# Kernel optimization log

Measured on AMD Instinct MI355X. Metric: run time of the kernel, lower is better.

Reference implementation:

```python
import jax, jax.numpy as jnp
import numpy as np

NBINS = 29
NODES = 5


def setup_inputs() -> dict:
    key = jax.random.key(0)
    ks = jax.random.split(key, 9)
    B, Tq, Td, V, H = 64, 32, 4096, 100000, 300
    sentence = jax.random.randint(ks[0], (B, Td), 0, V)
    query_sentence = jax.random.randint(ks[1], (B, Tq), 0, V)
    query_idf = jax.random.uniform(ks[2], (B, Tq), jnp.float32)
    emb = jax.random.normal(ks[3], (V, H), jnp.float32)
    w1 = jax.random.uniform(ks[4], (NBINS + 1, NODES), jnp.float32, -0.1, 0.1)
    b1 = jnp.zeros((NODES,), jnp.float32)
    w2 = jax.random.uniform(ks[5], (NODES, 1), jnp.float32, -0.1, 0.1)
    b2 = jnp.zeros((1,), jnp.float32)
    gate_w = jax.random.uniform(ks[6], (1,), jnp.float32, -0.01, 0.01)
    out_w = jax.random.normal(ks[7], (1, 1), jnp.float32) * 0.1
    out_b = jnp.zeros((1,), jnp.float32)
    return dict(sentence=sentence, query_sentence=query_sentence, query_idf=query_idf,
                emb=emb, w1=w1, b1=b1, w2=w2, b2=b2, gate_w=gate_w, out_w=out_w, out_b=out_b)


def reference(sentence, query_sentence, query_idf, emb, w1, b1, w2, b2, gate_w, out_w, out_b):
    B, Td = sentence.shape
    Tq = query_sentence.shape[1]
    q_mask = (query_sentence != 0).astype(jnp.float32)  # (B,Tq)
    d_mask = (sentence != 0).astype(jnp.float32)        # (B,Td)
    qx = emb[query_sentence]                            # (B,Tq,H)
    dx = emb[sentence]                                  # (B,Td,H)
    q_norm = jnp.sqrt(jnp.sum(qx * qx, -1) + 1e-7)[:, :, None] + 1e-7
    d_norm = jnp.sqrt(jnp.sum(dx * dx, -1) + 1e-7)[:, None, :] + 1e-7
    sim = jnp.einsum('bqh,bdh->bqd', qx, dx) / q_norm / d_norm  # (B,Tq,Td)
    sim = sim + (1.0 - d_mask)[:, None, :] * 1e7  # push masked doc positions out of all bins
    # Histogram: original does nbins cumulative (sim < ub) passes then a cumulative
    # subtraction; equivalent per-element bin index + one scatter-add pass.
    ubs = jnp.linspace(-1.0, 1.0, NBINS + 1)[1:]
    idx = jnp.searchsorted(ubs, sim, side='right')  # bin j <=> ub[j-1] <= sim < ub[j]; NBINS = out-of-range
    rows = jnp.arange(B * Tq)[:, None]
    counts = jnp.zeros((B * Tq, NBINS), jnp.float32).at[rows, idx.reshape(B * Tq, Td)].add(1.0, mode='drop')
    counts = counts.reshape(B, Tq, NBINS)
    exact = jnp.sum((sim > 0.999) & (sim < 1.001), axis=-1).astype(jnp.float32)  # exact-match bin
    hist = jnp.log(jnp.concatenate([counts, exact[..., None]], axis=-1) + 1.0)   # histType == 'LCH'
    ffw = jnp.tanh(jnp.tanh(hist @ w1 + b1) @ w2 + b2)[..., 0]  # (B,Tq)
    # gateType == 'IDF': Linear(1,1,bias=False) on idf, masked softmax over query terms
    gate_logits = query_idf * gate_w[0] + (1.0 - q_mask) * -1e7
    w = jax.nn.softmax(gate_logits, axis=1)
    x = jnp.sum(w * ffw, axis=-1, keepdims=True)  # (B,1)
    return x * out_w[0, 0] + out_b
```

## Files before the change

kernel.cpp:

```cpp
#include <hip/hip_runtime.h>
#include <hip/hip_bf16.h>
#include <math.h>

#define B_    64
#define TQ    32
#define TD    4096
#define HDIM  300
#define NB    29
#define NFEAT 30
#define NKT   19
#define THREADS 256
#define DPB   64
#define QF_SLOTS (NKT * 2 * 64)
#define QF_F4    (QF_SLOTS / 2)
#define QF_BYTES (QF_SLOTS * 8)

typedef _Float16 half4 __attribute__((ext_vector_type(4)));
typedef float    f32x4 __attribute__((ext_vector_type(4)));

__device__ __forceinline__ float ubf(int k) {
    return (float)(-1.0 + (2.0 * (double)(k + 1)) / 29.0);
}

__device__ __forceinline__ void bin_one(float sim, unsigned* s_hist, int q) {
    if (sim > 0.999f && sim < 1.001f) {
        atomicAdd(&s_hist[q * NFEAT + 28], 1u);
        atomicAdd(&s_hist[q * NFEAT + 29], 1u);
    } else {
        int idx = (int)((sim + 1.0f) * 14.5f);
        idx = idx < 0 ? 0 : (idx > NB ? NB : idx);
        while (idx < NB && sim >= ubf(idx)) ++idx;
        while (idx > 0 && sim < ubf(idx - 1)) --idx;
        if (idx < NB) atomicAdd(&s_hist[q * NFEAT + idx], 1u);
    }
}

__global__ void k_qfrag(const int* __restrict__ qsent, const float* __restrict__ emb,
                        _Float16* __restrict__ qf, float* __restrict__ invq) {
    const int b = blockIdx.x;
    const int t = threadIdx.x;
    const int row = t & 31, half = t >> 5;
    __shared__ float pn[2][TQ];
    const int tok = qsent[b * TQ + row];
    const float* p = emb + (size_t)tok * HDIM;
    _Float16* qfb = qf + (size_t)b * (QF_SLOTS * 4);
    float n = 0.f;
    for (int i = 0; i < 38; ++i) {
        const int jf = half * 38 + i;
        const int kg = jf * 4;
        float4 v = make_float4(0.f, 0.f, 0.f, 0.f);
        if (kg < 297) v = *(const float4*)(p + kg);
        n = fmaf(v.x, v.x, n); n = fmaf(v.y, v.y, n);
        n = fmaf(v.z, v.z, n); n = fmaf(v.w, v.w, n);
        half4 h = {(_Float16)v.x, (_Float16)v.y, (_Float16)v.z, (_Float16)v.w};
        const int kt = jf >> 2, g = jf & 3;
        const int slot = (kt * 2 + (row >> 4)) * 64 + (row & 15) + 16 * g;
        *(half4*)&qfb[slot * 4] = h;
    }
    pn[half][row] = n;
    __syncthreads();
    if (half == 0) {
        float s = pn[0][row] + pn[1][row];
        invq[b * TQ + row] = 1.0f / (sqrtf(s + 1e-7f) + 1e-7f);
    }
}

__global__ __launch_bounds__(THREADS) void k_main(
        const int* __restrict__ sent, const float* __restrict__ emb,
        const _Float16* __restrict__ qf, const float* __restrict__ invq,
        unsigned* __restrict__ ghist) {
    __shared__ __align__(16) _Float16 afr[QF_SLOTS * 4];
    __shared__ int      toks[DPB];
    __shared__ float    s_iq[TQ];
    __shared__ unsigned s_hist[TQ * NFEAT];

    const int b    = blockIdx.x >> 6;
    const int d0   = (blockIdx.x & 63) * DPB;
    const int tid  = threadIdx.x;
    const int wid  = tid >> 6;
    const int lane = tid & 63;

    if (tid < DPB) toks[tid] = sent[b * TD + d0 + tid];
    if (tid < TQ)  s_iq[tid] = invq[b * TQ + tid];
    for (int i = tid; i < TQ * NFEAT; i += THREADS) s_hist[i] = 0u;
    {
        const float4* qfp = (const float4*)(qf + (size_t)b * (QF_SLOTS * 4));
        float4* afp = (float4*)afr;
        for (int i = tid; i < QF_F4; i += THREADS) afp[i] = qfp[i];
    }
    __syncthreads();

    const int g4   = lane >> 4;
    const int rloc = wid * 16 + (lane & 15);
    const int tok  = toks[rloc];
    const float* bp = emb + (size_t)tok * HDIM + g4 * 4;

    f32x4 acc0 = {0.f, 0.f, 0.f, 0.f};
    f32x4 acc1 = {0.f, 0.f, 0.f, 0.f};
    float nd = 0.f;

    auto ldB = [&](int kt) -> float4 {
        if (kt == 18 && g4 == 3) return make_float4(0.f, 0.f, 0.f, 0.f);
        return *(const float4*)(bp + kt * 16);
    };

    float4 pre[6];
#pragma unroll
    for (int p = 0; p < 6; ++p) pre[p] = ldB(p);

#pragma unroll
    for (int kt = 0; kt < NKT; ++kt) {
        float4 v = pre[kt % 6];
        if (kt + 6 < NKT) pre[kt % 6] = ldB(kt + 6);
        nd = fmaf(v.x, v.x, nd); nd = fmaf(v.y, v.y, nd);
        nd = fmaf(v.z, v.z, nd); nd = fmaf(v.w, v.w, nd);
        half4 hb = {(_Float16)v.x, (_Float16)v.y, (_Float16)v.z, (_Float16)v.w};
        half4 a0 = *(const half4*)&afr[((kt * 2 + 0) * 64 + lane) * 4];
        half4 a1 = *(const half4*)&afr[((kt * 2 + 1) * 64 + lane) * 4];
        acc0 = __builtin_amdgcn_mfma_f32_16x16x16f16(a0, hb, acc0, 0, 0, 0);
        acc1 = __builtin_amdgcn_mfma_f32_16x16x16f16(a1, hb, acc1, 0, 0, 0);
    }

    float s = nd;
    s += __shfl_xor(s, 16, 64);
    s += __shfl_xor(s, 32, 64);
    const float idv = 1.0f / (sqrtf(s + 1e-7f) + 1e-7f);

    if (tok != 0) {
#pragma unroll
        for (int r = 0; r < 4; ++r) {
            const int q0 = g4 * 4 + r;
            bin_one(acc0[r] * s_iq[q0] * idv, s_hist, q0);
            const int q1 = 16 + g4 * 4 + r;
            bin_one(acc1[r] * s_iq[q1] * idv, s_hist, q1);
        }
    }
    __syncthreads();
    for (int i = tid; i < TQ * NFEAT; i += THREADS) {
        unsigned v = s_hist[i];
        if (v) atomicAdd(&ghist[b * TQ * NFEAT + i], v);
    }
}

__global__ void k_finish(const unsigned* __restrict__ ghist,
                         const int* __restrict__ qsent, const float* __restrict__ idf,
                         const float* __restrict__ w1, const float* __restrict__ b1,
                         const float* __restrict__ w2, const float* __restrict__ b2,
                         const float* __restrict__ gw, const float* __restrict__ ow,
                         const float* __restrict__ ob, float* __restrict__ out) {
    int b = blockIdx.x;
    int lane = threadIdx.x;
    float ffw = 0.f;
    float logit = -3.0e38f;
    if (lane < TQ) {
        const unsigned* h = ghist + (b * TQ + lane) * NFEAT;
        float f[NFEAT];
        for (int k = 0; k < NFEAT; ++k) f[k] = logf((float)h[k] + 1.0f);
        float s2 = b2[0];
        for (int n = 0; n < 5; ++n) {
            float s = b1[n];
            for (int k = 0; k < NFEAT; ++k) s = fmaf(f[k], w1[k * 5 + n], s);
            s2 = fmaf(tanhf(s), w2[n], s2);
        }
        ffw = tanhf(s2);
        int qt = qsent[b * TQ + lane];
        logit = idf[b * TQ + lane] * gw[0] + (qt == 0 ? -1e7f : 0.f);
    }
    float m = logit;
#pragma unroll
    for (int t = 1; t < 64; t <<= 1) m = fmaxf(m, __shfl_xor(m, t, 64));
    float e = expf(logit - m);
    float se = e, sw = e * ffw;
#pragma unroll
    for (int t = 1; t < 64; t <<= 1) {
        se += __shfl_xor(se, t, 64);
        sw += __shfl_xor(sw, t, 64);
    }
    if (lane == 0) out[b] = (sw / se) * ow[0] + ob[0];
}

extern "C" void kernel_launch(void* const* d_in, const int* in_sizes, int n_in,
                              void* d_out, int out_size, void* d_ws, size_t ws_size,
                              hipStream_t stream) {
    const int*   sent  = (const int*)d_in[0];
    const int*   qsent = (const int*)d_in[1];
    const float* idf   = (const float*)d_in[2];
    const float* emb   = (const float*)d_in[3];
    const float* w1    = (const float*)d_in[4];
    const float* b1    = (const float*)d_in[5];
    const float* w2    = (const float*)d_in[6];
    const float* b2    = (const float*)d_in[7];
    const float* gw    = (const float*)d_in[8];
    const float* ow    = (const float*)d_in[9];
    const float* ob    = (const float*)d_in[10];
    float* out = (float*)d_out;

    char* ws = (char*)d_ws;
    unsigned*  ghist = (unsigned*)ws;
    _Float16*  qfrag = (_Float16*)(ws + (256 << 10));
    float*     invq  = (float*)(ws + (256 << 10) + (size_t)B_ * QF_BYTES);

    hipMemsetAsync(ghist, 0, (size_t)B_ * TQ * NFEAT * 4, stream);
    k_qfrag<<<B_, 64, 0, stream>>>(qsent, emb, qfrag, invq);
    k_main<<<B_ * (TD / DPB), THREADS, 0, stream>>>(sent, emb, qfrag, invq, ghist);
    k_finish<<<B_, 64, 0, stream>>>(ghist, qsent, idf, w1, b1, w2, b2, gw, ow, ob, out);
}
```

Baseline: 96.32 us.

## Process two doc tile sets per warp and issue gathers before LDS setup

Each block now handles 128 document tokens instead of 64. Each wave processes two 16-row sets, so every LDS load of query fragments feeds twice as many MFMAs. Token ids are read directly from global memory, and the first embedding gathers are issued before the shared-memory histogram clear and query-fragment copy, so load latency overlaps that setup. This halves the grid size and the per-block setup and flush cost, at the price of doubled register use for prefetch buffers and accumulators, which may lower occupancy.

```diff
diff --git a/kernel.cpp b/kernel.cpp
--- a/kernel.cpp
+++ b/kernel.cpp
@@ -10,7 +10,9 @@
 #define NFEAT 30
 #define NKT   19
 #define THREADS 256
-#define DPB   64
+#define DPB   128
+#define NSET  2
+#define RDEP  6
 #define QF_SLOTS (NKT * 2 * 64)
 #define QF_F4    (QF_SLOTS / 2)
 #define QF_BYTES (QF_SLOTS * 8)
@@ -70,69 +72,85 @@
         const _Float16* __restrict__ qf, const float* __restrict__ invq,
         unsigned* __restrict__ ghist) {
     __shared__ __align__(16) _Float16 afr[QF_SLOTS * 4];
-    __shared__ int      toks[DPB];
     __shared__ float    s_iq[TQ];
     __shared__ unsigned s_hist[TQ * NFEAT];
 
-    const int b    = blockIdx.x >> 6;
-    const int d0   = (blockIdx.x & 63) * DPB;
+    const int b    = blockIdx.x >> 5;
+    const int d0   = (blockIdx.x & 31) * DPB;
     const int tid  = threadIdx.x;
     const int wid  = tid >> 6;
     const int lane = tid & 63;
 
-    if (tid < DPB) toks[tid] = sent[b * TD + d0 + tid];
-    if (tid < TQ)  s_iq[tid] = invq[b * TQ + tid];
+    const int g4   = lane >> 4;
+    const int r16  = lane & 15;
+    int tok[NSET];
+    const float* bp[NSET];
+#pragma unroll
+    for (int s = 0; s < NSET; ++s) {
+        tok[s] = sent[b * TD + d0 + wid * 16 + r16 + s * 64];
+        bp[s]  = emb + (size_t)tok[s] * HDIM + g4 * 4;
+    }
+
+    auto ldB = [&](int s, int kt) -> float4 {
+        if (kt == 18 && g4 == 3) return make_float4(0.f, 0.f, 0.f, 0.f);
+        return *(const float4*)(bp[s] + kt * 16);
+    };
+
+    float4 pre[NSET][RDEP];
+#pragma unroll
+    for (int p = 0; p < RDEP; ++p) {
+#pragma unroll
+        for (int s = 0; s < NSET; ++s) pre[s][p] = ldB(s, p);
+    }
+
     for (int i = tid; i < TQ * NFEAT; i += THREADS) s_hist[i] = 0u;
     {
         const float4* qfp = (const float4*)(qf + (size_t)b * (QF_SLOTS * 4));
         float4* afp = (float4*)afr;
         for (int i = tid; i < QF_F4; i += THREADS) afp[i] = qfp[i];
     }
+    if (tid < TQ) s_iq[tid] = invq[b * TQ + tid];
     __syncthreads();
 
-    const int g4   = lane >> 4;
-    const int rloc = wid * 16 + (lane & 15);
-    const int tok  = toks[rloc];
-    const float* bp = emb + (size_t)tok * HDIM + g4 * 4;
-
-    f32x4 acc0 = {0.f, 0.f, 0.f, 0.f};
-    f32x4 acc1 = {0.f, 0.f, 0.f, 0.f};
-    float nd = 0.f;
-
-    auto ldB = [&](int kt) -> float4 {
-        if (kt == 18 && g4 == 3) return make_float4(0.f, 0.f, 0.f, 0.f);
-        return *(const float4*)(bp + kt * 16);
-    };
-
-    float4 pre[6];
-#pragma unroll
-    for (int p = 0; p < 6; ++p) pre[p] = ldB(p);
+    f32x4 acc0[NSET], acc1[NSET];
+    float nd[NSET];
+#pragma unroll
+    for (int s = 0; s < NSET; ++s) {
+        acc0[s] = (f32x4){0.f, 0.f, 0.f, 0.f};
+        acc1[s] = (f32x4){0.f, 0.f, 0.f, 0.f};
+        nd[s] = 0.f;
+    }
 
 #pragma unroll
     for (int kt = 0; kt < NKT; ++kt) {
-        float4 v = pre[kt % 6];
-        if (kt + 6 < NKT) pre[kt % 6] = ldB(kt + 6);
-        nd = fmaf(v.x, v.x, nd); nd = fmaf(v.y, v.y, nd);
-        nd = fmaf(v.z, v.z, nd); nd = fmaf(v.w, v.w, nd);
-        half4 hb = {(_Float16)v.x, (_Float16)v.y, (_Float16)v.z, (_Float16)v.w};
         half4 a0 = *(const half4*)&afr[((kt * 2 + 0) * 64 + lane) * 4];
         half4 a1 = *(const half4*)&afr[((kt * 2 + 1) * 64 + lane) * 4];
-        acc0 = __builtin_amdgcn_mfma_f32_16x16x16f16(a0, hb, acc0, 0, 0, 0);
-        acc1 = __builtin_amdgcn_mfma_f32_16x16x16f16(a1, hb, acc1, 0, 0, 0);
-    }
-
-    float s = nd;
-    s += __shfl_xor(s, 16, 64);
-    s += __shfl_xor(s, 32, 64);
-    const float idv = 1.0f / (sqrtf(s + 1e-7f) + 1e-7f);
-
-    if (tok != 0) {
-#pragma unroll
-        for (int r = 0; r < 4; ++r) {
-            const int q0 = g4 * 4 + r;
-            bin_one(acc0[r] * s_iq[q0] * idv, s_hist, q0);
-            const int q1 = 16 + g4 * 4 + r;
-            bin_one(acc1[r] * s_iq[q1] * idv, s_hist, q1);
+#pragma unroll
+        for (int s = 0; s < NSET; ++s) {
+            float4 v = pre[s][kt % RDEP];
+            if (kt + RDEP < NKT) pre[s][kt % RDEP] = ldB(s, kt + RDEP);
+            nd[s] = fmaf(v.x, v.x, nd[s]); nd[s] = fmaf(v.y, v.y, nd[s]);
+            nd[s] = fmaf(v.z, v.z, nd[s]); nd[s] = fmaf(v.w, v.w, nd[s]);
+            half4 hb = {(_Float16)v.x, (_Float16)v.y, (_Float16)v.z, (_Float16)v.w};
+            acc0[s] = __builtin_amdgcn_mfma_f32_16x16x16f16(a0, hb, acc0[s], 0, 0, 0);
+            acc1[s] = __builtin_amdgcn_mfma_f32_16x16x16f16(a1, hb, acc1[s], 0, 0, 0);
+        }
+    }
+
+#pragma unroll
+    for (int s = 0; s < NSET; ++s) {
+        float t = nd[s];
+        t += __shfl_xor(t, 16, 64);
+        t += __shfl_xor(t, 32, 64);
+        const float idv = 1.0f / (sqrtf(t + 1e-7f) + 1e-7f);
+        if (tok[s] != 0) {
+#pragma unroll
+            for (int r = 0; r < 4; ++r) {
+                const int q0 = g4 * 4 + r;
+                bin_one(acc0[s][r] * s_iq[q0] * idv, s_hist, q0);
+                const int q1 = 16 + g4 * 4 + r;
+                bin_one(acc1[s][r] * s_iq[q1] * idv, s_hist, q1);
+            }
         }
     }
     __syncthreads();
```

Result: slower. 118.4 us (+22.9%).

## Process four doc chunks per block with cross-chunk prefetch and widen qfrag kernel

Applied to the files above, without the earlier changes.

Each main-kernel block now covers 256 document positions in four 64-row chunks instead of 64. The query fragment load into LDS, histogram clearing and global atomic flush are amortized over four times the work. The register prefetch ring continues across chunk boundaries, and the first embedding loads are issued before the LDS setup so they overlap it. The query-fragment kernel uses 256 threads with 8 segments to shorten its serial loop. The trade-off is fewer blocks (1024 vs 4096) and more registers per thread, which can lower occupancy.

```diff
diff --git a/kernel.cpp b/kernel.cpp
--- a/kernel.cpp
+++ b/kernel.cpp
@@ -10,7 +10,9 @@
 #define NFEAT 30
 #define NKT   19
 #define THREADS 256
-#define DPB   64
+#define NCH   4
+#define DPB   256
+#define RDEP  6
 #define QF_SLOTS (NKT * 2 * 64)
 #define QF_F4    (QF_SLOTS / 2)
 #define QF_BYTES (QF_SLOTS * 8)
@@ -39,29 +41,33 @@
                         _Float16* __restrict__ qf, float* __restrict__ invq) {
     const int b = blockIdx.x;
     const int t = threadIdx.x;
-    const int row = t & 31, half = t >> 5;
-    __shared__ float pn[2][TQ];
+    const int row = t & 31, seg = t >> 5;
+    __shared__ float pn[8][TQ];
     const int tok = qsent[b * TQ + row];
     const float* p = emb + (size_t)tok * HDIM;
     _Float16* qfb = qf + (size_t)b * (QF_SLOTS * 4);
     float n = 0.f;
-    for (int i = 0; i < 38; ++i) {
-        const int jf = half * 38 + i;
-        const int kg = jf * 4;
-        float4 v = make_float4(0.f, 0.f, 0.f, 0.f);
-        if (kg < 297) v = *(const float4*)(p + kg);
-        n = fmaf(v.x, v.x, n); n = fmaf(v.y, v.y, n);
-        n = fmaf(v.z, v.z, n); n = fmaf(v.w, v.w, n);
-        half4 h = {(_Float16)v.x, (_Float16)v.y, (_Float16)v.z, (_Float16)v.w};
-        const int kt = jf >> 2, g = jf & 3;
-        const int slot = (kt * 2 + (row >> 4)) * 64 + (row & 15) + 16 * g;
-        *(half4*)&qfb[slot * 4] = h;
-    }
-    pn[half][row] = n;
+#pragma unroll
+    for (int i = 0; i < 10; ++i) {
+        const int jf = seg * 10 + i;
+        if (jf < 76) {
+            const int kg = jf * 4;
+            float4 v = make_float4(0.f, 0.f, 0.f, 0.f);
+            if (kg < 297) v = *(const float4*)(p + kg);
+            n = fmaf(v.x, v.x, n); n = fmaf(v.y, v.y, n);
+            n = fmaf(v.z, v.z, n); n = fmaf(v.w, v.w, n);
+            half4 h = {(_Float16)v.x, (_Float16)v.y, (_Float16)v.z, (_Float16)v.w};
+            const int kt = jf >> 2, g = jf & 3;
+            const int slot = (kt * 2 + (row >> 4)) * 64 + (row & 15) + 16 * g;
+            *(half4*)&qfb[slot * 4] = h;
+        }
+    }
+    pn[seg][row] = n;
     __syncthreads();
-    if (half == 0) {
-        float s = pn[0][row] + pn[1][row];
-        invq[b * TQ + row] = 1.0f / (sqrtf(s + 1e-7f) + 1e-7f);
+    if (t < TQ) {
+        float s = ((pn[0][t] + pn[1][t]) + (pn[2][t] + pn[3][t]))
+                + ((pn[4][t] + pn[5][t]) + (pn[6][t] + pn[7][t]));
+        invq[b * TQ + t] = 1.0f / (sqrtf(s + 1e-7f) + 1e-7f);
     }
 }
 
@@ -70,69 +76,75 @@
         const _Float16* __restrict__ qf, const float* __restrict__ invq,
         unsigned* __restrict__ ghist) {
     __shared__ __align__(16) _Float16 afr[QF_SLOTS * 4];
-    __shared__ int      toks[DPB];
     __shared__ float    s_iq[TQ];
     __shared__ unsigned s_hist[TQ * NFEAT];
 
-    const int b    = blockIdx.x >> 6;
-    const int d0   = (blockIdx.x & 63) * DPB;
+    const int b    = blockIdx.x >> 4;
+    const int d0   = (blockIdx.x & 15) * DPB;
     const int tid  = threadIdx.x;
     const int wid  = tid >> 6;
     const int lane = tid & 63;
 
-    if (tid < DPB) toks[tid] = sent[b * TD + d0 + tid];
-    if (tid < TQ)  s_iq[tid] = invq[b * TQ + tid];
+    const int g4   = lane >> 4;
+    const int r16  = lane & 15;
+
+    int tok[NCH];
+    const float* bp[NCH];
+#pragma unroll
+    for (int ch = 0; ch < NCH; ++ch) {
+        tok[ch] = sent[b * TD + d0 + ch * 64 + wid * 16 + r16];
+        bp[ch]  = emb + (size_t)tok[ch] * HDIM + g4 * 4;
+    }
+
+    auto ldBg = [&](int g) -> float4 {
+        const int ch = g / NKT, kt = g - ch * NKT;
+        if (kt == 18 && g4 == 3) return make_float4(0.f, 0.f, 0.f, 0.f);
+        return *(const float4*)(bp[ch] + kt * 16);
+    };
+
+    float4 pre[RDEP];
+#pragma unroll
+    for (int p = 0; p < RDEP; ++p) pre[p] = ldBg(p);
+
     for (int i = tid; i < TQ * NFEAT; i += THREADS) s_hist[i] = 0u;
     {
         const float4* qfp = (const float4*)(qf + (size_t)b * (QF_SLOTS * 4));
         float4* afp = (float4*)afr;
         for (int i = tid; i < QF_F4; i += THREADS) afp[i] = qfp[i];
     }
+    if (tid < TQ) s_iq[tid] = invq[b * TQ + tid];
     __syncthreads();
 
-    const int g4   = lane >> 4;
-    const int rloc = wid * 16 + (lane & 15);
-    const int tok  = toks[rloc];
-    const float* bp = emb + (size_t)tok * HDIM + g4 * 4;
-
-    f32x4 acc0 = {0.f, 0.f, 0.f, 0.f};
-    f32x4 acc1 = {0.f, 0.f, 0.f, 0.f};
-    float nd = 0.f;
-
-    auto ldB = [&](int kt) -> float4 {
-        if (kt == 18 && g4 == 3) return make_float4(0.f, 0.f, 0.f, 0.f);
-        return *(const float4*)(bp + kt * 16);
-    };
-
-    float4 pre[6];
-#pragma unroll
-    for (int p = 0; p < 6; ++p) pre[p] = ldB(p);
-
-#pragma unroll
-    for (int kt = 0; kt < NKT; ++kt) {
-        float4 v = pre[kt % 6];
-        if (kt + 6 < NKT) pre[kt % 6] = ldB(kt + 6);
-        nd = fmaf(v.x, v.x, nd); nd = fmaf(v.y, v.y, nd);
-        nd = fmaf(v.z, v.z, nd); nd = fmaf(v.w, v.w, nd);
-        half4 hb = {(_Float16)v.x, (_Float16)v.y, (_Float16)v.z, (_Float16)v.w};
-        half4 a0 = *(const half4*)&afr[((kt * 2 + 0) * 64 + lane) * 4];
-        half4 a1 = *(const half4*)&afr[((kt * 2 + 1) * 64 + lane) * 4];
-        acc0 = __builtin_amdgcn_mfma_f32_16x16x16f16(a0, hb, acc0, 0, 0, 0);
-        acc1 = __builtin_amdgcn_mfma_f32_16x16x16f16(a1, hb, acc1, 0, 0, 0);
-    }
-
-    float s = nd;
-    s += __shfl_xor(s, 16, 64);
-    s += __shfl_xor(s, 32, 64);
-    const float idv = 1.0f / (sqrtf(s + 1e-7f) + 1e-7f);
-
-    if (tok != 0) {
-#pragma unroll
-        for (int r = 0; r < 4; ++r) {
-            const int q0 = g4 * 4 + r;
-            bin_one(acc0[r] * s_iq[q0] * idv, s_hist, q0);
-            const int q1 = 16 + g4 * 4 + r;
-            bin_one(acc1[r] * s_iq[q1] * idv, s_hist, q1);
+#pragma unroll
+    for (int ch = 0; ch < NCH; ++ch) {
+        f32x4 acc0 = {0.f, 0.f, 0.f, 0.f};
+        f32x4 acc1 = {0.f, 0.f, 0.f, 0.f};
+        float nd = 0.f;
+#pragma unroll
+        for (int kt = 0; kt < NKT; ++kt) {
+            const int g = ch * NKT + kt;
+            float4 v = pre[g % RDEP];
+            if (g + RDEP < NCH * NKT) pre[g % RDEP] = ldBg(g + RDEP);
+            nd = fmaf(v.x, v.x, nd); nd = fmaf(v.y, v.y, nd);
+            nd = fmaf(v.z, v.z, nd); nd = fmaf(v.w, v.w, nd);
+            half4 hb = {(_Float16)v.x, (_Float16)v.y, (_Float16)v.z, (_Float16)v.w};
+            half4 a0 = *(const half4*)&afr[((kt * 2 + 0) * 64 + lane) * 4];
+            half4 a1 = *(const half4*)&afr[((kt * 2 + 1) * 64 + lane) * 4];
+            acc0 = __builtin_amdgcn_mfma_f32_16x16x16f16(a0, hb, acc0, 0, 0, 0);
+            acc1 = __builtin_amdgcn_mfma_f32_16x16x16f16(a1, hb, acc1, 0, 0, 0);
+        }
+        float t = nd;
+        t += __shfl_xor(t, 16, 64);
+        t += __shfl_xor(t, 32, 64);
+        const float idv = 1.0f / (sqrtf(t + 1e-7f) + 1e-7f);
+        if (tok[ch] != 0) {
+#pragma unroll
+            for (int r = 0; r < 4; ++r) {
+                const int q0 = g4 * 4 + r;
+                bin_one(acc0[r] * s_iq[q0] * idv, s_hist, q0);
+                const int q1 = 16 + g4 * 4 + r;
+                bin_one(acc1[r] * s_iq[q1] * idv, s_hist, q1);
+            }
         }
     }
     __syncthreads();
@@ -201,7 +213,7 @@
     float*     invq  = (float*)(ws + (256 << 10) + (size_t)B_ * QF_BYTES);
 
     hipMemsetAsync(ghist, 0, (size_t)B_ * TQ * NFEAT * 4, stream);
-    k_qfrag<<<B_, 64, 0, stream>>>(qsent, emb, qfrag, invq);
+    k_qfrag<<<B_, 256, 0, stream>>>(qsent, emb, qfrag, invq);
     k_main<<<B_ * (TD / DPB), THREADS, 0, stream>>>(sent, emb, qfrag, invq, ghist);
     k_finish<<<B_, 64, 0, stream>>>(ghist, qsent, idf, w1, b1, w2, b2, gw, ow, ob, out);
 }
```

After: 91.92 us. 1.05x faster.
